# Optimization experiments

Measured on AMD Instinct MI355X. Metric: run time of the kernel, lower is better.

## Reference

```python
import jax, jax.numpy as jnp
import numpy as np

KERNEL_SIZE = 3


def extract_local_features(feature_map, point_coords, kernel_size=KERNEL_SIZE):
    # feature_map: (B,C,H,W); point_coords: (B,N,2) normalized (y,x) in [0,1]
    B, C, H, W = feature_map.shape
    half = kernel_size // 2
    x = (point_coords[..., 1] * (W - 1)).astype(jnp.int32)  # (B,N)
    y = (point_coords[..., 0] * (H - 1)).astype(jnp.int32)
    x_min = jnp.clip(x - half, 0, None)
    x_max = jnp.clip(x + half + 1, None, W)
    y_min = jnp.clip(y - half, 0, None)
    y_max = jnpp_clip = jnp.clip(y + half + 1, None, H)
    y_max = jnp.clip(y + half + 1, None, H)
    # gather a fixed (k,k) window with clamped offsets, mask out-of-window entries
    offs = jnp.arange(kernel_size)  # (k,)
    yy = y_min[..., None] + offs  # (B,N,k) candidate rows
    xx = x_min[..., None] + offs  # (B,N,k)
    y_valid = yy < y_max[..., None]
    x_valid = xx < x_max[..., None]
    yy_c = jnp.clip(yy, 0, H - 1)
    xx_c = jnp.clip(xx, 0, W - 1)
    # flat spatial indices (B,N,k,k)
    flat_idx = yy_c[..., :, None] * W + xx_c[..., None, :]
    valid = (y_valid[..., :, None] & x_valid[..., None, :]).astype(feature_map.dtype)
    fm_flat = feature_map.reshape(B, C, H * W)  # (B,C,HW)

    def per_batch(fm, idx, val):
        # fm: (C,HW); idx,val: (N,k,k)
        g = fm[:, idx.reshape(-1)].reshape(fm.shape[0], *idx.shape)  # (C,N,k,k)
        s = jnp.einsum('cnij,nij->cn', g, val)
        cnt = val.sum(axis=(-1, -2))  # (N,)
        return s / cnt[None, :]

    return jax.vmap(per_batch)(fm_flat, flat_idx, valid)  # (B,C,N)


def point_sample(inp, point_coords):
    # bilinear grid_sample, align_corners=False, coords in [0,1] as (x,y) order
    # per the code: grid = 2*coords - 1; grid_sample uses (x,y) convention
    B, C, H, W = inp.shape
    gx = point_coords[..., 0]  # (B,N) in [0,1]
    gy = point_coords[..., 1]
    # align_corners=False mapping: pix = ((g*2-1)+1)/2 * size - 0.5 = g*size - 0.5
    fx = gx * W - 0.5
    fy = gy * H - 0.5
    x0 = jnp.floor(fx).astype(jnp.int32)
    y0 = jnp.floor(fy).astype(jnp.int32)
    wx = fx - x0
    wy = fy - y0

    def gather(yc, xc):
        inb = ((yc >= 0) & (yc < H) & (xc >= 0) & (xc < W)).astype(inp.dtype)  # (B,N)
        ycc = jnp.clip(yc, 0, H - 1)
        xcc = jnp.clip(xc, 0, W - 1)
        flat = ycc * W + xcc  # (B,N)
        fm = inp.reshape(B, C, H * W)
        g = jax.vmap(lambda f, i: f[:, i])(fm, flat)  # (B,C,N)
        return g * inb[:, None, :]

    v00 = gather(y0, x0)
    v01 = gather(y0, x0 + 1)
    v10 = gather(y0 + 1, x0)
    v11 = gather(y0 + 1, x0 + 1)
    wx_ = wx[:, None, :]
    wy_ = wy[:, None, :]
    out = (v00 * (1 - wx_) * (1 - wy_) + v01 * wx_ * (1 - wy_)
           + v10 * (1 - wx_) * wy_ + v11 * wx_ * wy_)  # (B,C,N)
    return out.transpose(0, 2, 1)  # (B,N,C)


def calculate_uncertainty(mask_logits):
    return -jnp.abs(mask_logits).squeeze(1)  # (B,H,W)


def edge_topk_sampling(edge_masks, uncertainty_map, topk):
    # edge_masks: (B,H,W) {0,1}; uncertainty_map: (B,H,W)
    B, H, W = edge_masks.shape
    NEG = jnp.asarray(-1e30, uncertainty_map.dtype)
    masked_u = jnp.where(edge_masks.reshape(B, -1) == 1,
                         uncertainty_map.reshape(B, -1), NEG)
    vals, idx = jax.lax.top_k(masked_u, topk)  # (B,topk)
    yi = (idx // W).astype(jnp.float32)
    xi = (idx % W).astype(jnp.float32)
    coords = jnp.stack([yi / (H - 1), xi / (W - 1)], axis=-1)  # (B,topk,2) (y,x)
    return idx, coords


def setup_inputs() -> dict:
    key = jax.random.key(0)
    k1, k2, k3, k4 = jax.random.split(key, 4)
    B, C, H, W = 8, 256, 256, 256
    N = 4096
    feature_map = jax.random.normal(k1, (B, C, H, W), dtype=jnp.float32)
    pred_mask = jax.random.normal(k2, (B, 1, H, W), dtype=jnp.float32)
    edge_masks = jax.random.randint(k3, (B, H, W), 0, 2).astype(jnp.int32)
    point_coords = jax.random.uniform(k4, (B, N, 2), dtype=jnp.float32)
    return {"feature_map": feature_map, "pred_mask": pred_mask,
            "edge_masks": edge_masks, "point_coords": point_coords,
            "topk": 4096}


def reference(feature_map, pred_mask, edge_masks, point_coords, topk):
    uncertainty_map = calculate_uncertainty(pred_mask)  # (B,H,W)
    idx, important_coords = edge_topk_sampling(edge_masks, uncertainty_map, topk)
    local_feats = extract_local_features(feature_map, important_coords)  # (B,C,topk)
    sampled = point_sample(feature_map, point_coords)  # (B,N,C)
    return local_feats, sampled, important_coords, idx
```

## Files before the change

kernel.cpp:

```cpp
#include <hip/hip_runtime.h>

#define CC 256
#define HH 256
#define WW 256
#define HWV 65536
#define NN 4096

using u64 = unsigned long long;
using u32 = unsigned int;

__global__ void build_keys_k(const float* __restrict__ pm, const int* __restrict__ em,
                             u64* __restrict__ keys) {
    int i = blockIdx.x * blockDim.x + threadIdx.x;
    float f = (em[i] == 1) ? -fabsf(pm[i]) : -1e30f;
    u32 u = __float_as_uint(f);
    u32 k = (u & 0x80000000u) ? ~u : (u | 0x80000000u);
    u32 pix = (u32)i & 0xFFFFu;
    keys[i] = ((u64)k << 16) | (u64)(0xFFFFu - pix);
}

template<int DIRECT>
__global__ __launch_bounds__(1024) void topk_sortpc_k(const u64* __restrict__ keys,
                                                      const float* __restrict__ pc,
                                                      u32* __restrict__ stash,
                                                      u32* __restrict__ pixSorted,
                                                      u32* __restrict__ pcSorted,
                                                      float* __restrict__ outCoord,
                                                      float* __restrict__ outIdx) {
    __shared__ u64 sel[NN];
    __shared__ u64 bm[1024];
    __shared__ u32 wp[1024];
    __shared__ u32 s_digit, s_rem, s_cnt;
    const int t = threadIdx.x;
    if (blockIdx.x < 8) {
        const int b = blockIdx.x;
        const u64* kb = keys + (size_t)b * HWV;
        u32* hist = (u32*)sel;
        u64 prefix = 0ULL;
        u32 remaining = NN;
        for (int r = 0; r < 4; ++r) {
            int shift = 36 - 12 * r;
            #pragma unroll
            for (int q = 0; q < 4; ++q) hist[t + q * 1024] = 0u;
            __syncthreads();
            for (int i = t; i < HWV; i += 1024) {
                u64 K = kb[i];
                if ((K >> (shift + 12)) == prefix)
                    atomicAdd(&hist[(u32)((K >> shift) & 0xFFFULL)], 1u);
            }
            __syncthreads();
            for (int off = 1; off < 4096; off <<= 1) {
                u32 v[4];
                #pragma unroll
                for (int q = 0; q < 4; ++q) {
                    int i = t + q * 1024;
                    v[q] = hist[i];
                    if (i + off < 4096) v[q] += hist[i + off];
                }
                __syncthreads();
                #pragma unroll
                for (int q = 0; q < 4; ++q) hist[t + q * 1024] = v[q];
                __syncthreads();
            }
            #pragma unroll
            for (int q = 0; q < 4; ++q) {
                int d = t + q * 1024;
                u32 ge = hist[d];
                u32 gt = (d < 4095) ? hist[d + 1] : 0u;
                if (ge >= remaining && gt < remaining) { s_digit = (u32)d; s_rem = remaining - gt; }
            }
            __syncthreads();
            prefix = (prefix << 12) | (u64)s_digit;
            remaining = s_rem;
            __syncthreads();
        }
        if (t == 0) s_cnt = 0u;
        __syncthreads();
        for (int i = t; i < HWV; i += 1024) {
            u64 K = kb[i];
            if (K >= prefix) { u32 p = atomicAdd(&s_cnt, 1u); sel[p] = K; }
        }
        __syncthreads();
        for (int k = 2; k <= NN; k <<= 1) {
            for (int j = k >> 1; j > 0; j >>= 1) {
                for (int i = t; i < NN; i += 1024) {
                    int l = i ^ j;
                    if (l > i) {
                        u64 a = sel[i], c = sel[l];
                        bool asc = ((i & k) == 0);
                        if ((a < c) == asc) { sel[i] = c; sel[l] = a; }
                    }
                }
                __syncthreads();
            }
        }
        bm[t] = 0ULL;
        __syncthreads();
        #pragma unroll
        for (int q = 0; q < 4; ++q) {
            int r = t + q * 1024;
            u32 pix = 0xFFFFu - (u32)(sel[r] & 0xFFFFULL);
            if (DIRECT) {
                u32 yi = pix >> 8, xi = pix & 255u;
                outCoord[((size_t)b * NN + r) * 2 + 0] = (float)yi / 255.0f;
                outCoord[((size_t)b * NN + r) * 2 + 1] = (float)xi / 255.0f;
                outIdx[b * NN + r] = (float)pix;
            } else {
                stash[b * NN + r] = pix;
            }
            atomicOr(&bm[pix >> 6], 1ULL << (pix & 63));
        }
        __syncthreads();
        wp[t] = (u32)__popcll(bm[t]);
        __syncthreads();
        for (int off = 1; off < 1024; off <<= 1) {
            u32 v = wp[t];
            if (t >= off) v += wp[t - off];
            __syncthreads();
            wp[t] = v;
            __syncthreads();
        }
        #pragma unroll
        for (int q = 0; q < 4; ++q) {
            int r = t + q * 1024;
            u32 pix = 0xFFFFu - (u32)(sel[r] & 0xFFFFULL);
            int w = (int)(pix >> 6);
            u32 pos = wp[w] - (u32)__popcll(bm[w])
                    + (u32)__popcll(bm[w] & ((1ULL << (pix & 63)) - 1ULL));
            pixSorted[b * NN + pos] = (pix << 12) | (u32)r;
        }
    } else {
        const int b = blockIdx.x - 8;
        u32* cellArr = (u32*)sel;
        u32* hist256 = wp;
        u32* cnt     = (u32*)bm;
        if (t < 256) { hist256[t] = 0u; cnt[t] = 0u; }
        __syncthreads();
        for (int n = t; n < NN; n += 1024) {
            float gx = pc[((size_t)b * NN + n) * 2 + 0];
            float gy = pc[((size_t)b * NN + n) * 2 + 1];
            float fx = gx * 256.0f - 0.5f;
            float fy = gy * 256.0f - 0.5f;
            int x0 = (int)floorf(fx), y0 = (int)floorf(fy);
            int xc = min(max(x0, 0), 255), yc = min(max(y0, 0), 255);
            cellArr[n] = ((u32)(yc * 256 + xc) << 12) | (u32)n;
            atomicAdd(&hist256[yc], 1u);
        }
        __syncthreads();
        for (int off = 1; off < 256; off <<= 1) {
            u32 v = 0;
            if (t < 256) { v = hist256[t]; if (t >= off) v += hist256[t - off]; }
            __syncthreads();
            if (t < 256) hist256[t] = v;
            __syncthreads();
        }
        for (int n = t; n < NN; n += 1024) {
            u32 pk = cellArr[n];
            u32 yc = pk >> 20;
            u32 base = (yc > 0) ? hist256[yc - 1] : 0u;
            u32 pos = base + atomicAdd(&cnt[yc], 1u);
            pcSorted[b * NN + pos] = pk;
        }
    }
}

template<int MODE>
__global__ __launch_bounds__(256, 4) void gather_k(const float* __restrict__ fm,
                                                   const float* __restrict__ pc,
                                                   const u32* __restrict__ pixSorted,
                                                   const u32* __restrict__ pcSorted,
                                                   float* __restrict__ outLp,
                                                   float* __restrict__ outS) {
    __shared__ float tile[256][33];
    __shared__ u32 pidx[256];
    const int b = blockIdx.z, j0 = blockIdx.x * 256, t = threadIdx.x;
    bool doL; int c0;
    if (MODE == 0) { doL = (blockIdx.y < 8); c0 = (doL ? blockIdx.y : blockIdx.y - 8) * 32; }
    else if (MODE == 1) { doL = true; c0 = blockIdx.y * 32; }
    else { doL = false; c0 = blockIdx.y * 32; }
    const float* planes = fm + ((size_t)b * CC + c0) * HWV;

    if (doL) {
        u32 packed = pixSorted[b * NN + j0 + t];
        u32 pix = packed >> 12;
        pidx[t] = packed & 0xFFFu;
        int yi = (int)(pix >> 8), xi = (int)(pix & 255u);
        float cy = (float)yi / 255.0f;
        float cx = (float)xi / 255.0f;
        int x = (int)(cx * 255.0f);
        int y = (int)(cy * 255.0f);
        int x_min = max(x - 1, 0), x_max = min(x + 2, WW);
        int y_min = max(y - 1, 0), y_max = min(y + 2, HH);
        int base = min(x_min & ~3, WW - 8);
        float w8[8];
        #pragma unroll
        for (int i = 0; i < 8; ++i)
            w8[i] = (base + i >= x_min && base + i < x_max) ? 1.0f : 0.0f;
        float wr2 = (y_min + 2 < y_max) ? 1.0f : 0.0f;
        int o0 = y_min * WW + base;
        int o1 = o0 + WW;
        int o2 = min(y_min + 2, HH - 1) * WW + base;
        float invc = 1.0f / (float)((x_max - x_min) * (y_max - y_min));
        #pragma unroll 2
        for (int j = 0; j < 32; ++j) {
            const float* p = planes + (size_t)j * HWV;
            float4 a0 = *(const float4*)(p + o0);
            float4 b0 = *(const float4*)(p + o0 + 4);
            float4 a1 = *(const float4*)(p + o1);
            float4 b1 = *(const float4*)(p + o1 + 4);
            float4 a2 = *(const float4*)(p + o2);
            float4 b2 = *(const float4*)(p + o2 + 4);
            float s0 = a0.x * w8[0] + a0.y * w8[1] + a0.z * w8[2] + a0.w * w8[3]
                     + b0.x * w8[4] + b0.y * w8[5] + b0.z * w8[6] + b0.w * w8[7];
            float s1 = a1.x * w8[0] + a1.y * w8[1] + a1.z * w8[2] + a1.w * w8[3]
                     + b1.x * w8[4] + b1.y * w8[5] + b1.z * w8[6] + b1.w * w8[7];
            float s2 = a2.x * w8[0] + a2.y * w8[1] + a2.z * w8[2] + a2.w * w8[3]
                     + b2.x * w8[4] + b2.y * w8[5] + b2.z * w8[6] + b2.w * w8[7];
            tile[t][j] = (s0 + s1 + wr2 * s2) * invc;
        }
        __syncthreads();
        for (int idx = t; idx < 8192; idx += 256) {
            int p = idx >> 5, k = idx & 31;
            outLp[((size_t)b * NN + pidx[p]) * CC + c0 + k] = tile[p][k];
        }
    } else {
        int n = (int)(pcSorted[b * NN + j0 + t] & 0xFFFu);
        pidx[t] = (u32)n;
        float gx = pc[((size_t)b * NN + n) * 2 + 0];
        float gy = pc[((size_t)b * NN + n) * 2 + 1];
        float fx = gx * 256.0f - 0.5f;
        float fy = gy * 256.0f - 0.5f;
        float fx0 = floorf(fx), fy0 = floorf(fy);
        int x0 = (int)fx0, y0 = (int)fy0;
        float wx = fx - fx0, wy = fy - fy0;
        int xb = min(max(x0, 0), WW - 2);
        float wv0, wv1;
        if (x0 < 0)            { wv0 = wx;        wv1 = 0.0f; }
        else if (x0 >= WW - 1) { wv0 = 0.0f;      wv1 = 1.0f - wx; }
        else                   { wv0 = 1.0f - wx; wv1 = wx; }
        float wr0 = (y0 >= 0)     ? (1.0f - wy) : 0.0f;
        float wr1 = (y0 + 1 < HH) ? wy          : 0.0f;
        int yc0 = min(max(y0, 0), HH - 1);
        int yc1 = min(max(y0 + 1, 0), HH - 1);
        int o0 = yc0 * WW + xb;
        int o1 = yc1 * WW + xb;
        #pragma unroll 4
        for (int j = 0; j < 32; ++j) {
            const float* p = planes + (size_t)j * HWV;
            tile[t][j] = wr0 * (p[o0] * wv0 + p[o0 + 1] * wv1)
                       + wr1 * (p[o1] * wv0 + p[o1 + 1] * wv1);
        }
        __syncthreads();
        for (int idx = t; idx < 8192; idx += 256) {
            int p = idx >> 5, k = idx & 31;
            outS[((size_t)b * NN + pidx[p]) * CC + c0 + k] = tile[p][k];
        }
    }
}

__global__ __launch_bounds__(256) void transpose_k(const float* __restrict__ outLp,
                                                   float* __restrict__ outL) {
    __shared__ float tile[256][33];
    const int b = blockIdx.z, c0 = blockIdx.y * 32, r0 = blockIdx.x * 256;
    const int t = threadIdx.x;
    for (int idx = t; idx < 8192; idx += 256) {
        int p = idx >> 5, k = idx & 31;
        tile[p][k] = outLp[((size_t)b * NN + r0 + p) * CC + c0 + k];
    }
    __syncthreads();
    for (int idx = t; idx < 8192; idx += 256) {
        int cl = idx >> 8, col = idx & 255;
        outL[((size_t)b * CC + c0 + cl) * NN + r0 + col] = tile[col][cl];
    }
}

__global__ void emit_k(const u32* __restrict__ stash, float* __restrict__ outCoord,
                       float* __restrict__ outIdx) {
    int i = blockIdx.x * blockDim.x + threadIdx.x;
    u32 p = stash[i];
    u32 yi = p >> 8, xi = p & 255u;
    outCoord[(size_t)i * 2 + 0] = (float)yi / 255.0f;
    outCoord[(size_t)i * 2 + 1] = (float)xi / 255.0f;
    outIdx[i] = (float)p;
}

extern "C" void kernel_launch(void* const* d_in, const int* in_sizes, int n_in,
                              void* d_out, int out_size, void* d_ws, size_t ws_size,
                              hipStream_t stream) {
    const float* fm = (const float*)d_in[0];
    const float* pm = (const float*)d_in[1];
    const int*   em = (const int*)d_in[2];
    const float* pc = (const float*)d_in[3];
    (void)in_sizes; (void)n_in; (void)out_size;

    float* out      = (float*)d_out;
    float* outL     = out;
    float* outS     = out + (size_t)8388608;
    float* outCoord = out + (size_t)16777216;
    float* outIdx   = out + (size_t)16842752;

    const size_t need_ws = (size_t)40 * 1024 * 1024;
    bool ws_ok = ws_size >= need_ws;

    u64* keys; u32 *stash, *pixSorted, *pcSorted; float* outLp;
    if (ws_ok) {
        char* w = (char*)d_ws;
        keys      = (u64*)w;
        stash     = (u32*)(w + (size_t)4  * 1024 * 1024);
        pixSorted = (u32*)(w + (size_t)4300 * 1024);
        pcSorted  = (u32*)(w + (size_t)4600 * 1024);
        outLp     = (float*)(w + (size_t)5 * 1024 * 1024);
    } else {
        keys      = (u64*)outS;
        stash     = (u32*)outIdx;
        pixSorted = (u32*)outCoord;
        pcSorted  = pixSorted + 32768;
        outLp     = outS;
    }

    hipLaunchKernelGGL(build_keys_k, dim3(2048), dim3(256), 0, stream, pm, em, keys);
    if (ws_ok) {
        hipLaunchKernelGGL((topk_sortpc_k<1>), dim3(16), dim3(1024), 0, stream,
                           keys, pc, stash, pixSorted, pcSorted, outCoord, outIdx);
        hipLaunchKernelGGL((gather_k<0>), dim3(16, 16, 8), dim3(256), 0, stream,
                           fm, pc, pixSorted, pcSorted, outLp, outS);
        hipLaunchKernelGGL(transpose_k, dim3(16, 8, 8), dim3(256), 0, stream, outLp, outL);
    } else {
        hipLaunchKernelGGL((topk_sortpc_k<0>), dim3(16), dim3(1024), 0, stream,
                           keys, pc, stash, pixSorted, pcSorted, outCoord, outIdx);
        hipLaunchKernelGGL((gather_k<1>), dim3(16, 8, 8), dim3(256), 0, stream,
                           fm, pc, pixSorted, pcSorted, outLp, outS);
        hipLaunchKernelGGL(transpose_k, dim3(16, 8, 8), dim3(256), 0, stream, outLp, outL);
        hipLaunchKernelGGL((gather_k<2>), dim3(16, 8, 8), dim3(256), 0, stream,
                           fm, pc, pixSorted, pcSorted, outS, outS);
        hipLaunchKernelGGL(emit_k, dim3(128), dim3(256), 0, stream, stash, outCoord, outIdx);
    }
}
```

Measured before the change: 324.3 us.

## Stage 16-row feature-plane bands in LDS and gather sorted points from shared memory

```diff
diff --git a/kernel.cpp b/kernel.cpp
--- a/kernel.cpp
+++ b/kernel.cpp
@@ -5,9 +5,17 @@
 #define WW 256
 #define HWV 65536
 #define NN 4096
+#define SROWS 18
+#define SSTRIDE 260
 
 using u64 = unsigned long long;
 using u32 = unsigned int;
+
+__device__ __forceinline__ u32 lbound(const u32* __restrict__ a, u32 n, u32 key) {
+    u32 lo = 0, hi = n;
+    while (lo < hi) { u32 mid = (lo + hi) >> 1; if (a[mid] < key) lo = mid + 1; else hi = mid; }
+    return lo;
+}
 
 __global__ void build_keys_k(const float* __restrict__ pm, const int* __restrict__ em,
                              u64* __restrict__ keys) {
@@ -164,6 +172,222 @@
     }
 }
 
+#define STAGE_LOAD(plane) \
+    { int idx, r, c4, gr; \
+      idx = t;        r = idx >> 6; c4 = idx & 63; gr = min(max(rStart + r, 0), HH - 1); \
+      g0 = *(const float4*)((plane) + gr * WW + c4 * 4); \
+      idx = t + 256;  r = idx >> 6; c4 = idx & 63; gr = min(max(rStart + r, 0), HH - 1); \
+      g1 = *(const float4*)((plane) + gr * WW + c4 * 4); \
+      idx = t + 512;  r = idx >> 6; c4 = idx & 63; gr = min(max(rStart + r, 0), HH - 1); \
+      g2 = *(const float4*)((plane) + gr * WW + c4 * 4); \
+      idx = t + 768;  r = idx >> 6; c4 = idx & 63; gr = min(max(rStart + r, 0), HH - 1); \
+      g3 = *(const float4*)((plane) + gr * WW + c4 * 4); \
+      if (t < 128) { idx = t + 1024; r = idx >> 6; c4 = idx & 63; gr = min(max(rStart + r, 0), HH - 1); \
+      g4 = *(const float4*)((plane) + gr * WW + c4 * 4); } }
+
+#define STAGE_WRITE() \
+    { int idx, r, c4; \
+      idx = t;        r = idx >> 6; c4 = idx & 63; *(float4*)(sm + r * SSTRIDE + c4 * 4) = g0; \
+      idx = t + 256;  r = idx >> 6; c4 = idx & 63; *(float4*)(sm + r * SSTRIDE + c4 * 4) = g1; \
+      idx = t + 512;  r = idx >> 6; c4 = idx & 63; *(float4*)(sm + r * SSTRIDE + c4 * 4) = g2; \
+      idx = t + 768;  r = idx >> 6; c4 = idx & 63; *(float4*)(sm + r * SSTRIDE + c4 * 4) = g3; \
+      if (t < 128) { idx = t + 1024; r = idx >> 6; c4 = idx & 63; *(float4*)(sm + r * SSTRIDE + c4 * 4) = g4; } }
+
+__global__ __launch_bounds__(256) void plane_gather_k(const float* __restrict__ fm,
+                                                      const float* __restrict__ pc,
+                                                      const u32* __restrict__ pixSorted,
+                                                      const u32* __restrict__ pcSorted,
+                                                      float* __restrict__ outLc,
+                                                      float* __restrict__ outSc) {
+    __shared__ float sm[SROWS * SSTRIDE];
+    const int band = blockIdx.x, c0 = blockIdx.y * 32, b = blockIdx.z;
+    const int t = threadIdx.x;
+    const int rStart = band * 16 - 1;
+    const u32 keyLo = (u32)band << 24, keyHi = (u32)(band + 1) << 24;
+    const u32* aL = pixSorted + b * NN;
+    const u32* aS = pcSorted + b * NN;
+    u32 loL = lbound(aL, NN, keyLo), cL = lbound(aL, NN, keyHi) - loL;
+    u32 loS = lbound(aS, NN, keyLo), cS = lbound(aS, NN, keyHi) - loS;
+    const float* planes = fm + ((size_t)b * CC + c0) * HWV;
+    const float* pcb = pc + (size_t)b * NN * 2;
+
+    int  Lo0 = 0, Lc2 = 0, Lr2 = 0;   float Lwc = 0, Lwr = 0, Lic = 0;
+    int  Mo0 = 0, Mc2 = 0, Mr2 = 0;   float Mwc = 0, Mwr = 0, Mic = 0;
+    int  So0 = 0, Sr1 = 0;            float Sv0 = 0, Sv1 = 0, Sw0 = 0, Sw1 = 0;
+    int  To0 = 0, Tr1 = 0;            float Tv0 = 0, Tv1 = 0, Tw0 = 0, Tw1 = 0;
+    {
+        u32 jl = (u32)t;
+        if (jl < cL) {
+            u32 pix = aL[loL + jl] >> 12;
+            int yi = (int)(pix >> 8), xi = (int)(pix & 255u);
+            float cy = (float)yi / 255.0f, cx = (float)xi / 255.0f;
+            int x = (int)(cx * 255.0f), y = (int)(cy * 255.0f);
+            int x_min = max(x - 1, 0), wid = min(x + 2, WW) - x_min;
+            int y_min = max(y - 1, 0), hgt = min(y + 2, HH) - y_min;
+            Lo0 = (y_min - rStart) * SSTRIDE + x_min;
+            Lc2 = (wid == 3) ? 2 : 0;  Lwc = (wid == 3) ? 1.0f : 0.0f;
+            Lr2 = ((hgt == 3) ? 2 : 0) * SSTRIDE;  Lwr = (hgt == 3) ? 1.0f : 0.0f;
+            Lic = 1.0f / (float)(wid * hgt);
+        }
+        jl = 256u + (u32)t;
+        if (jl < cL) {
+            u32 pix = aL[loL + jl] >> 12;
+            int yi = (int)(pix >> 8), xi = (int)(pix & 255u);
+            float cy = (float)yi / 255.0f, cx = (float)xi / 255.0f;
+            int x = (int)(cx * 255.0f), y = (int)(cy * 255.0f);
+            int x_min = max(x - 1, 0), wid = min(x + 2, WW) - x_min;
+            int y_min = max(y - 1, 0), hgt = min(y + 2, HH) - y_min;
+            Mo0 = (y_min - rStart) * SSTRIDE + x_min;
+            Mc2 = (wid == 3) ? 2 : 0;  Mwc = (wid == 3) ? 1.0f : 0.0f;
+            Mr2 = ((hgt == 3) ? 2 : 0) * SSTRIDE;  Mwr = (hgt == 3) ? 1.0f : 0.0f;
+            Mic = 1.0f / (float)(wid * hgt);
+        }
+        u32 js = (u32)t;
+        if (js < cS) {
+            u32 sn = aS[loS + js] & 0xFFFu;
+            float gx = pcb[2 * sn + 0], gy = pcb[2 * sn + 1];
+            float fx = gx * 256.0f - 0.5f, fy = gy * 256.0f - 0.5f;
+            float fx0 = floorf(fx), fy0 = floorf(fy);
+            int x0 = (int)fx0, y0 = (int)fy0;
+            float wx = fx - fx0, wy = fy - fy0;
+            int xb = min(max(x0, 0), WW - 2);
+            if (x0 < 0)            { Sv0 = wx;        Sv1 = 0.0f; }
+            else if (x0 >= WW - 1) { Sv0 = 0.0f;      Sv1 = 1.0f - wx; }
+            else                   { Sv0 = 1.0f - wx; Sv1 = wx; }
+            Sw0 = (y0 >= 0)     ? (1.0f - wy) : 0.0f;
+            Sw1 = (y0 + 1 < HH) ? wy          : 0.0f;
+            int yc0 = min(max(y0, 0), HH - 1), yc1 = min(max(y0 + 1, 0), HH - 1);
+            So0 = (yc0 - rStart) * SSTRIDE + xb;
+            Sr1 = (yc1 - yc0) * SSTRIDE;
+        }
+        js = 256u + (u32)t;
+        if (js < cS) {
+            u32 sn = aS[loS + js] & 0xFFFu;
+            float gx = pcb[2 * sn + 0], gy = pcb[2 * sn + 1];
+            float fx = gx * 256.0f - 0.5f, fy = gy * 256.0f - 0.5f;
+            float fx0 = floorf(fx), fy0 = floorf(fy);
+            int x0 = (int)fx0, y0 = (int)fy0;
+            float wx = fx - fx0, wy = fy - fy0;
+            int xb = min(max(x0, 0), WW - 2);
+            if (x0 < 0)            { Tv0 = wx;        Tv1 = 0.0f; }
+            else if (x0 >= WW - 1) { Tv0 = 0.0f;      Tv1 = 1.0f - wx; }
+            else                   { Tv0 = 1.0f - wx; Tv1 = wx; }
+            Tw0 = (y0 >= 0)     ? (1.0f - wy) : 0.0f;
+            Tw1 = (y0 + 1 < HH) ? wy          : 0.0f;
+            int yc0 = min(max(y0, 0), HH - 1), yc1 = min(max(y0 + 1, 0), HH - 1);
+            To0 = (yc0 - rStart) * SSTRIDE + xb;
+            Tr1 = (yc1 - yc0) * SSTRIDE;
+        }
+    }
+
+    float4 g0, g1, g2, g3, g4;
+    STAGE_LOAD(planes)
+    STAGE_WRITE()
+    __syncthreads();
+
+    #pragma unroll 1
+    for (int j = 0; j < 32; ++j) {
+        if (j + 1 < 32) { const float* np = planes + (size_t)(j + 1) * HWV; STAGE_LOAD(np) }
+        float* oL = outLc + ((size_t)(b * CC + c0 + j)) * NN + loL;
+        float* oS = outSc + ((size_t)(b * CC + c0 + j)) * NN + loS;
+        if ((u32)t < cL) {
+            float r0 = sm[Lo0] + sm[Lo0 + 1] + Lwc * sm[Lo0 + Lc2];
+            float r1 = sm[Lo0 + SSTRIDE] + sm[Lo0 + SSTRIDE + 1] + Lwc * sm[Lo0 + SSTRIDE + Lc2];
+            int o2 = Lo0 + Lr2;
+            float r2 = sm[o2] + sm[o2 + 1] + Lwc * sm[o2 + Lc2];
+            oL[t] = (r0 + r1 + Lwr * r2) * Lic;
+        }
+        if (256u + (u32)t < cL) {
+            float r0 = sm[Mo0] + sm[Mo0 + 1] + Mwc * sm[Mo0 + Mc2];
+            float r1 = sm[Mo0 + SSTRIDE] + sm[Mo0 + SSTRIDE + 1] + Mwc * sm[Mo0 + SSTRIDE + Mc2];
+            int o2 = Mo0 + Mr2;
+            float r2 = sm[o2] + sm[o2 + 1] + Mwc * sm[o2 + Mc2];
+            oL[256 + t] = (r0 + r1 + Mwr * r2) * Mic;
+        }
+        if ((u32)t < cS) {
+            oS[t] = Sw0 * (sm[So0] * Sv0 + sm[So0 + 1] * Sv1)
+                  + Sw1 * (sm[So0 + Sr1] * Sv0 + sm[So0 + Sr1 + 1] * Sv1);
+        }
+        if (256u + (u32)t < cS) {
+            oS[256 + t] = Tw0 * (sm[To0] * Tv0 + sm[To0 + 1] * Tv1)
+                        + Tw1 * (sm[To0 + Tr1] * Tv0 + sm[To0 + Tr1 + 1] * Tv1);
+        }
+        __syncthreads();
+        if (j + 1 < 32) { STAGE_WRITE() }
+        __syncthreads();
+    }
+
+    for (u32 jl = 512 + (u32)t; jl < cL; jl += 256) {
+        u32 pix = aL[loL + jl] >> 12;
+        int yi = (int)(pix >> 8), xi = (int)(pix & 255u);
+        float cy = (float)yi / 255.0f, cx = (float)xi / 255.0f;
+        int x = (int)(cx * 255.0f), y = (int)(cy * 255.0f);
+        int x_min = max(x - 1, 0), x_max = min(x + 2, WW);
+        int y_min = max(y - 1, 0), y_max = min(y + 2, HH);
+        float ic = 1.0f / (float)((x_max - x_min) * (y_max - y_min));
+        for (int j = 0; j < 32; ++j) {
+            const float* p = planes + (size_t)j * HWV;
+            float s = 0.0f;
+            for (int yy = y_min; yy < y_max; ++yy)
+                for (int xx = x_min; xx < x_max; ++xx) s += p[yy * WW + xx];
+            outLc[((size_t)(b * CC + c0 + j)) * NN + loL + jl] = s * ic;
+        }
+    }
+    for (u32 js = 512 + (u32)t; js < cS; js += 256) {
+        u32 sn = aS[loS + js] & 0xFFFu;
+        float gx = pcb[2 * sn + 0], gy = pcb[2 * sn + 1];
+        float fx = gx * 256.0f - 0.5f, fy = gy * 256.0f - 0.5f;
+        float fx0 = floorf(fx), fy0 = floorf(fy);
+        int x0 = (int)fx0, y0 = (int)fy0;
+        float wx = fx - fx0, wy = fy - fy0;
+        int xb = min(max(x0, 0), WW - 2);
+        float v0, v1, r0, r1;
+        if (x0 < 0)            { v0 = wx;        v1 = 0.0f; }
+        else if (x0 >= WW - 1) { v0 = 0.0f;      v1 = 1.0f - wx; }
+        else                   { v0 = 1.0f - wx; v1 = wx; }
+        r0 = (y0 >= 0)     ? (1.0f - wy) : 0.0f;
+        r1 = (y0 + 1 < HH) ? wy          : 0.0f;
+        int yc0 = min(max(y0, 0), HH - 1), yc1 = min(max(y0 + 1, 0), HH - 1);
+        int o0 = yc0 * WW + xb, o1 = yc1 * WW + xb;
+        for (int j = 0; j < 32; ++j) {
+            const float* p = planes + (size_t)j * HWV;
+            outSc[((size_t)(b * CC + c0 + j)) * NN + loS + js] =
+                r0 * (p[o0] * v0 + p[o0 + 1] * v1) + r1 * (p[o1] * v0 + p[o1 + 1] * v1);
+        }
+    }
+}
+
+__global__ __launch_bounds__(256) void unpermL_k(const float* __restrict__ outLc,
+                                                 const u32* __restrict__ pixSorted,
+                                                 float* __restrict__ outL) {
+    __shared__ float row[NN];
+    const int c = blockIdx.x, b = blockIdx.y;
+    const int t = threadIdx.x;
+    const float* in = outLc + ((size_t)(b * CC + c)) * NN;
+    for (int j = t; j < NN; j += 256)
+        row[pixSorted[b * NN + j] & 0xFFFu] = in[j];
+    __syncthreads();
+    float* o = outL + ((size_t)(b * CC + c)) * NN;
+    for (int i = t; i < NN; i += 256) o[i] = row[i];
+}
+
+__global__ __launch_bounds__(256) void unpermS_k(const float* __restrict__ outSc,
+                                                 const u32* __restrict__ pcSorted,
+                                                 float* __restrict__ outS) {
+    __shared__ float tile[32][257];
+    __shared__ u32 ns[256];
+    const int j0 = blockIdx.x * 256, c0 = blockIdx.y * 32, b = blockIdx.z;
+    const int t = threadIdx.x;
+    ns[t] = pcSorted[b * NN + j0 + t] & 0xFFFu;
+    for (int i = 0; i < 32; ++i)
+        tile[i][t] = outSc[((size_t)(b * CC + c0 + i)) * NN + j0 + t];
+    __syncthreads();
+    for (int idx = t; idx < 8192; idx += 256) {
+        int p = idx >> 5, k = idx & 31;
+        outS[((size_t)b * NN + ns[p]) * CC + c0 + k] = tile[k][p];
+    }
+}
+
 template<int MODE>
 __global__ __launch_bounds__(256, 4) void gather_k(const float* __restrict__ fm,
                                                    const float* __restrict__ pc,
@@ -175,20 +399,16 @@
     __shared__ u32 pidx[256];
     const int b = blockIdx.z, j0 = blockIdx.x * 256, t = threadIdx.x;
     bool doL; int c0;
-    if (MODE == 0) { doL = (blockIdx.y < 8); c0 = (doL ? blockIdx.y : blockIdx.y - 8) * 32; }
-    else if (MODE == 1) { doL = true; c0 = blockIdx.y * 32; }
+    if (MODE == 1) { doL = true; c0 = blockIdx.y * 32; }
     else { doL = false; c0 = blockIdx.y * 32; }
     const float* planes = fm + ((size_t)b * CC + c0) * HWV;
-
     if (doL) {
         u32 packed = pixSorted[b * NN + j0 + t];
         u32 pix = packed >> 12;
         pidx[t] = packed & 0xFFFu;
         int yi = (int)(pix >> 8), xi = (int)(pix & 255u);
-        float cy = (float)yi / 255.0f;
-        float cx = (float)xi / 255.0f;
-        int x = (int)(cx * 255.0f);
-        int y = (int)(cy * 255.0f);
+        float cy = (float)yi / 255.0f, cx = (float)xi / 255.0f;
+        int x = (int)(cx * 255.0f), y = (int)(cy * 255.0f);
         int x_min = max(x - 1, 0), x_max = min(x + 2, WW);
         int y_min = max(y - 1, 0), y_max = min(y + 2, HH);
         int base = min(x_min & ~3, WW - 8);
@@ -197,19 +417,15 @@
         for (int i = 0; i < 8; ++i)
             w8[i] = (base + i >= x_min && base + i < x_max) ? 1.0f : 0.0f;
         float wr2 = (y_min + 2 < y_max) ? 1.0f : 0.0f;
-        int o0 = y_min * WW + base;
-        int o1 = o0 + WW;
+        int o0 = y_min * WW + base, o1 = o0 + WW;
         int o2 = min(y_min + 2, HH - 1) * WW + base;
         float invc = 1.0f / (float)((x_max - x_min) * (y_max - y_min));
         #pragma unroll 2
         for (int j = 0; j < 32; ++j) {
             const float* p = planes + (size_t)j * HWV;
-            float4 a0 = *(const float4*)(p + o0);
-            float4 b0 = *(const float4*)(p + o0 + 4);
-            float4 a1 = *(const float4*)(p + o1);
-            float4 b1 = *(const float4*)(p + o1 + 4);
-            float4 a2 = *(const float4*)(p + o2);
-            float4 b2 = *(const float4*)(p + o2 + 4);
+            float4 a0 = *(const float4*)(p + o0), b0 = *(const float4*)(p + o0 + 4);
+            float4 a1 = *(const float4*)(p + o1), b1 = *(const float4*)(p + o1 + 4);
+            float4 a2 = *(const float4*)(p + o2), b2 = *(const float4*)(p + o2 + 4);
             float s0 = a0.x * w8[0] + a0.y * w8[1] + a0.z * w8[2] + a0.w * w8[3]
                      + b0.x * w8[4] + b0.y * w8[5] + b0.z * w8[6] + b0.w * w8[7];
             float s1 = a1.x * w8[0] + a1.y * w8[1] + a1.z * w8[2] + a1.w * w8[3]
@@ -228,8 +444,7 @@
         pidx[t] = (u32)n;
         float gx = pc[((size_t)b * NN + n) * 2 + 0];
         float gy = pc[((size_t)b * NN + n) * 2 + 1];
-        float fx = gx * 256.0f - 0.5f;
-        float fy = gy * 256.0f - 0.5f;
+        float fx = gx * 256.0f - 0.5f, fy = gy * 256.0f - 0.5f;
         float fx0 = floorf(fx), fy0 = floorf(fy);
         int x0 = (int)fx0, y0 = (int)fy0;
         float wx = fx - fx0, wy = fy - fy0;
@@ -240,10 +455,8 @@
         else                   { wv0 = 1.0f - wx; wv1 = wx; }
         float wr0 = (y0 >= 0)     ? (1.0f - wy) : 0.0f;
         float wr1 = (y0 + 1 < HH) ? wy          : 0.0f;
-        int yc0 = min(max(y0, 0), HH - 1);
-        int yc1 = min(max(y0 + 1, 0), HH - 1);
-        int o0 = yc0 * WW + xb;
-        int o1 = yc1 * WW + xb;
+        int yc0 = min(max(y0, 0), HH - 1), yc1 = min(max(y0 + 1, 0), HH - 1);
+        int o0 = yc0 * WW + xb, o1 = yc1 * WW + xb;
         #pragma unroll 4
         for (int j = 0; j < 32; ++j) {
             const float* p = planes + (size_t)j * HWV;
@@ -299,33 +512,34 @@
     float* outCoord = out + (size_t)16777216;
     float* outIdx   = out + (size_t)16842752;
 
-    const size_t need_ws = (size_t)40 * 1024 * 1024;
+    const size_t need_ws = (size_t)80 * 1024 * 1024;
     bool ws_ok = ws_size >= need_ws;
 
-    u64* keys; u32 *stash, *pixSorted, *pcSorted; float* outLp;
     if (ws_ok) {
         char* w = (char*)d_ws;
-        keys      = (u64*)w;
-        stash     = (u32*)(w + (size_t)4  * 1024 * 1024);
-        pixSorted = (u32*)(w + (size_t)4300 * 1024);
-        pcSorted  = (u32*)(w + (size_t)4600 * 1024);
-        outLp     = (float*)(w + (size_t)5 * 1024 * 1024);
+        u64* keys      = (u64*)w;
+        u32* pixSorted = (u32*)(w + (size_t)4300 * 1024);
+        u32* pcSorted  = (u32*)(w + (size_t)4600 * 1024);
+        float* outLc   = (float*)(w + (size_t)5  * 1024 * 1024);
+        float* outSc   = (float*)(w + (size_t)40 * 1024 * 1024);
+
+        hipLaunchKernelGGL(build_keys_k, dim3(2048), dim3(256), 0, stream, pm, em, keys);
+        hipLaunchKernelGGL((topk_sortpc_k<1>), dim3(16), dim3(1024), 0, stream,
+                           keys, pc, (u32*)nullptr, pixSorted, pcSorted, outCoord, outIdx);
+        hipLaunchKernelGGL(plane_gather_k, dim3(16, 8, 8), dim3(256), 0, stream,
+                           fm, pc, pixSorted, pcSorted, outLc, outSc);
+        hipLaunchKernelGGL(unpermL_k, dim3(256, 8), dim3(256), 0, stream,
+                           outLc, pixSorted, outL);
+        hipLaunchKernelGGL(unpermS_k, dim3(16, 8, 8), dim3(256), 0, stream,
+                           outSc, pcSorted, outS);
     } else {
-        keys      = (u64*)outS;
-        stash     = (u32*)outIdx;
-        pixSorted = (u32*)outCoord;
-        pcSorted  = pixSorted + 32768;
-        outLp     = outS;
-    }
-
-    hipLaunchKernelGGL(build_keys_k, dim3(2048), dim3(256), 0, stream, pm, em, keys);
-    if (ws_ok) {
-        hipLaunchKernelGGL((topk_sortpc_k<1>), dim3(16), dim3(1024), 0, stream,
-                           keys, pc, stash, pixSorted, pcSorted, outCoord, outIdx);
-        hipLaunchKernelGGL((gather_k<0>), dim3(16, 16, 8), dim3(256), 0, stream,
-                           fm, pc, pixSorted, pcSorted, outLp, outS);
-        hipLaunchKernelGGL(transpose_k, dim3(16, 8, 8), dim3(256), 0, stream, outLp, outL);
-    } else {
+        u64* keys      = (u64*)outS;
+        u32* stash     = (u32*)outIdx;
+        u32* pixSorted = (u32*)outCoord;
+        u32* pcSorted  = pixSorted + 32768;
+        float* outLp   = outS;
+
+        hipLaunchKernelGGL(build_keys_k, dim3(2048), dim3(256), 0, stream, pm, em, keys);
         hipLaunchKernelGGL((topk_sortpc_k<0>), dim3(16), dim3(1024), 0, stream,
                            keys, pc, stash, pixSorted, pcSorted, outCoord, outIdx);
         hipLaunchKernelGGL((gather_k<1>), dim3(16, 8, 8), dim3(256), 0, stream,
```

Result: no change. 325.2 us (+0.3%).
